# Performance work log

Measured on AMD Instinct MI355X. Metric: run time of the kernel, lower is better.

## Reference

```python
import jax, jax.numpy as jnp
import numpy as np

TAB_DIM = 6
C = 64
B, X, Y, Z = 2, 64, 64, 64
EPS = float(np.finfo(np.float32).eps)


def _gauss_1d(mu, sigma, size):
    # mu, sigma: (B, C) -> mask (B, C, size)
    coords = jnp.arange(size, dtype=jnp.float32)  # (size,)
    mu = mu * (size / 2.0) + (size / 2.0) - 0.5
    sigma = sigma * 3.5 + EPS
    d = (coords[None, None, :] - mu[:, :, None]) / sigma[:, :, None]
    return jnp.exp(-0.5 * d * d)


def _frob(t):
    return jnp.sqrt(jnp.sum(t * t))


def setup_inputs() -> dict:
    key = jax.random.key(0)
    ks = jax.random.split(key, 10)
    h = C // 2
    def lin(k, fan_in, fan_out):
        bound = 1.0 / np.sqrt(fan_in)
        kw, kb = jax.random.split(k)
        w = jax.random.uniform(kw, (fan_out, fan_in), jnp.float32, -bound, bound)
        b = jax.random.uniform(kb, (fan_out,), jnp.float32, -bound, bound)
        return w, b
    w1, b1 = lin(ks[0], TAB_DIM, h)
    w2, b2 = lin(ks[1], h, h)
    wp, bp = lin(ks[2], h, 5 * C)
    ws, bs = lin(ks[3], h, 3 * C)
    x = jax.random.normal(ks[4], (B, C, X, Y, Z), jnp.float32)
    tab = jax.random.normal(ks[5], (B, TAB_DIM), jnp.float32)
    return {"x": x, "tab": tab, "w1": w1, "b1": b1, "w2": w2, "b2": b2,
            "wp": wp, "bp": bp, "ws": ws, "bs": bs}


def reference(x, tab, w1, b1, w2, b2, wp, bp, ws, bs):
    # hypernetwork (tiny MLPs)
    emb = jnp.tanh(tab @ w1.T + b1)
    emb = jnp.tanh(emb @ w2.T + b2)
    p = emb @ wp.T + bp                     # (B, 5C)
    s = jax.nn.sigmoid(emb @ ws.T + bs)     # (B, 3C)
    scale = p[..., :C]
    shift = p[..., C:2 * C]
    mu_a = jnp.tanh(p[..., 2 * C:3 * C])
    mu_b = jnp.tanh(p[..., 3 * C:4 * C])
    mu_c = jnp.tanh(p[..., 4 * C:])
    sigma_a = s[..., :C]
    sigma_b = s[..., C:2 * C]
    sigma_c = s[..., 2 * C:]

    l2 = _frob(scale) + _frob(shift) + _frob(sigma_a) + _frob(sigma_b) + _frob(sigma_c)

    _, _, sx, sy, sz = x.shape
    gx = _gauss_1d(mu_a, sigma_a, sx)  # (B, C, X)
    gy = _gauss_1d(mu_b, sigma_b, sy)  # (B, C, Y)
    gz = _gauss_1d(mu_c, sigma_c, sz)  # (B, C, Z)

    # rank-1 outer product over X,Y,Z == the chained matmuls in torch
    a = gx[:, :, :, None, None] * gy[:, :, None, :, None] * gz[:, :, None, None, :]

    out = (1.0 - scale)[:, :, None, None, None] * x * a + shift[:, :, None, None, None]
    return out, l2
```

## Files before the change

### kernel.cpp

```cpp
#include <hip/hip_runtime.h>
#include <math.h>

#define EPSF 1.1920929e-07f

typedef float f4 __attribute__((ext_vector_type(4)));

__device__ __forceinline__ float sigmoidf_(float v) { return 1.0f / (1.0f + expf(-v)); }

__global__ void __launch_bounds__(256) fused_kernel(
        const float* __restrict__ xin, const float* __restrict__ tab,
        const float* __restrict__ w1,  const float* __restrict__ b1,
        const float* __restrict__ w2,  const float* __restrict__ b2,
        const float* __restrict__ wp,  const float* __restrict__ bp,
        const float* __restrict__ wsg, const float* __restrict__ bsg,
        float* __restrict__ out, int out_last)
{
    __shared__ float emb1[2][32];
    __shared__ float emb2[2][32];
    __shared__ float head[8];
    __shared__ float gys[64], gzs[64];
    __shared__ float pv_sh, sh_sh;

    const int blk = blockIdx.x;
    const int bc  = blk >> 6;
    const int xi  = blk & 63;
    const int b   = bc >> 6;
    const int c   = bc & 63;
    const int tid = threadIdx.x;

    if (tid < 64) {
        int bb = tid >> 5, j = tid & 31;
        float acc = b1[j];
        #pragma unroll
        for (int k = 0; k < 6; ++k) acc += tab[bb * 6 + k] * w1[j * 6 + k];
        emb1[bb][j] = tanhf(acc);
    }
    __syncthreads();

    if (tid < 64) {
        int bb = tid >> 5, j = tid & 31;
        float acc = b2[j];
        #pragma unroll
        for (int k = 0; k < 32; ++k) acc += emb1[bb][k] * w2[j * 32 + k];
        emb2[bb][j] = tanhf(acc);
    }
    __syncthreads();

    if (tid < 8) {
        const float* W  = (tid < 5) ? wp  : wsg;
        const float* Bv = (tid < 5) ? bp  : bsg;
        int row = ((tid < 5) ? tid : (tid - 5)) * 64 + c;
        float acc = Bv[row];
        #pragma unroll
        for (int k = 0; k < 32; ++k) acc += emb2[b][k] * W[row * 32 + k];
        head[tid] = acc;
    }
    __syncthreads();

    if (tid < 64) {
        float m  = tanhf(head[3]) * 32.0f + 31.5f;
        float sg = sigmoidf_(head[6]) * 3.5f + EPSF;
        float d  = ((float)tid - m) / sg;
        gys[tid] = expf(-0.5f * d * d);
    } else if (tid < 128) {
        int i = tid - 64;
        float m  = tanhf(head[4]) * 32.0f + 31.5f;
        float sg = sigmoidf_(head[7]) * 3.5f + EPSF;
        float d  = ((float)i - m) / sg;
        gzs[i] = expf(-0.5f * d * d);
    } else if (tid == 128) {
        float m  = tanhf(head[2]) * 32.0f + 31.5f;
        float sg = sigmoidf_(head[5]) * 3.5f + EPSF;
        float d  = ((float)xi - m) / sg;
        pv_sh = (1.0f - head[0]) * expf(-0.5f * d * d);
        sh_sh = head[1];
    }

    if (blk == 0) {
        __shared__ float sq[5][128];
        for (int t = tid; t < 640; t += 256) {
            int q = t / 128, r = t % 128;
            int bb = r >> 6, cc = r & 63;
            const float* W  = (q < 2) ? wp  : wsg;
            const float* Bv = (q < 2) ? bp  : bsg;
            int row = ((q < 2) ? q : (q - 2)) * 64 + cc;
            float acc = Bv[row];
            #pragma unroll
            for (int k = 0; k < 32; ++k) acc += emb2[bb][k] * W[row * 32 + k];
            if (q >= 2) acc = sigmoidf_(acc);
            sq[q][r] = acc * acc;
        }
        __syncthreads();
        if (tid == 0) {
            float tot = 0.0f;
            for (int q = 0; q < 5; ++q) {
                float ssum = 0.0f;
                for (int i = 0; i < 128; ++i) ssum += sq[q][i];
                tot += sqrtf(ssum);
            }
            out[out_last] = tot;
        }
    }
    __syncthreads();

    const float pv = pv_sh;
    const float sh = sh_sh;
    const f4* x4 = (const f4*)(xin + (size_t)blk * 4096);
    f4*       o4 = (f4*)(out + (size_t)blk * 4096);

    #pragma unroll
    for (int k = 0; k < 4; ++k) {
        int i4 = tid + k * 256;
        int y  = i4 >> 4;
        int z0 = (i4 & 15) << 2;
        f4 xv = __builtin_nontemporal_load(&x4[i4]);
        float m = pv * gys[y];
        f4 ov;
        ov.x = fmaf(m * gzs[z0 + 0], xv.x, sh);
        ov.y = fmaf(m * gzs[z0 + 1], xv.y, sh);
        ov.z = fmaf(m * gzs[z0 + 2], xv.z, sh);
        ov.w = fmaf(m * gzs[z0 + 3], xv.w, sh);
        __builtin_nontemporal_store(ov, &o4[i4]);
    }
}

extern "C" void kernel_launch(void* const* d_in, const int* in_sizes, int n_in,
                              void* d_out, int out_size, void* d_ws, size_t ws_size,
                              hipStream_t stream)
{
    const float* x   = (const float*)d_in[0];
    const float* tab = (const float*)d_in[1];
    const float* w1  = (const float*)d_in[2];
    const float* b1  = (const float*)d_in[3];
    const float* w2  = (const float*)d_in[4];
    const float* b2  = (const float*)d_in[5];
    const float* wp  = (const float*)d_in[6];
    const float* bp  = (const float*)d_in[7];
    const float* wsg = (const float*)d_in[8];
    const float* bsg = (const float*)d_in[9];

    float* out = (float*)d_out;

    fused_kernel<<<2 * 64 * 64, 256, 0, stream>>>(
        x, tab, w1, b1, w2, b2, wp, bp, wsg, bsg, out, out_size - 1);
}
```

Baseline: 49.48 us.

## Split hypernetwork setup into separate kernel and precompute gaussian tables

```diff
diff --git a/kernel.cpp b/kernel.cpp
--- a/kernel.cpp
+++ b/kernel.cpp
@@ -7,24 +7,23 @@
 
 __device__ __forceinline__ float sigmoidf_(float v) { return 1.0f / (1.0f + expf(-v)); }
 
-__global__ void __launch_bounds__(256) fused_kernel(
-        const float* __restrict__ xin, const float* __restrict__ tab,
+__global__ void __launch_bounds__(256) setup_kernel(
+        const float* __restrict__ tab,
         const float* __restrict__ w1,  const float* __restrict__ b1,
         const float* __restrict__ w2,  const float* __restrict__ b2,
         const float* __restrict__ wp,  const float* __restrict__ bp,
         const float* __restrict__ wsg, const float* __restrict__ bsg,
+        float* __restrict__ pvt, float* __restrict__ sht,
+        f4* __restrict__ gy4T, f4* __restrict__ gz4t,
         float* __restrict__ out, int out_last)
 {
     __shared__ float emb1[2][32];
     __shared__ float emb2[2][32];
     __shared__ float head[8];
     __shared__ float gys[64], gzs[64];
-    __shared__ float pv_sh, sh_sh;
 
-    const int blk = blockIdx.x;
-    const int bc  = blk >> 6;
-    const int xi  = blk & 63;
-    const int b   = bc >> 6;
+    const int bc  = blockIdx.x;
+    const int b   = (bc >> 6) & 1;
     const int c   = bc & 63;
     const int tid = threadIdx.x;
 
@@ -45,6 +44,33 @@
         emb2[bb][j] = tanhf(acc);
     }
     __syncthreads();
+
+    if (bc == 128) {
+        __shared__ float sq[5][128];
+        for (int t = tid; t < 640; t += 256) {
+            int q = t / 128, r = t % 128;
+            int bb = r >> 6, cc = r & 63;
+            const float* W  = (q < 2) ? wp  : wsg;
+            const float* Bv = (q < 2) ? bp  : bsg;
+            int row = ((q < 2) ? q : (q - 2)) * 64 + cc;
+            float acc = Bv[row];
+            #pragma unroll
+            for (int k = 0; k < 32; ++k) acc += emb2[bb][k] * W[row * 32 + k];
+            if (q >= 2) acc = sigmoidf_(acc);
+            sq[q][r] = acc * acc;
+        }
+        __syncthreads();
+        if (tid == 0) {
+            float tot = 0.0f;
+            for (int q = 0; q < 5; ++q) {
+                float ssum = 0.0f;
+                for (int i = 0; i < 128; ++i) ssum += sq[q][i];
+                tot += sqrtf(ssum);
+            }
+            out[out_last] = tot;
+        }
+        return;
+    }
 
     if (tid < 8) {
         const float* W  = (tid < 5) ? wp  : wsg;
@@ -68,60 +94,60 @@
         float sg = sigmoidf_(head[7]) * 3.5f + EPSF;
         float d  = ((float)i - m) / sg;
         gzs[i] = expf(-0.5f * d * d);
-    } else if (tid == 128) {
-        float m  = tanhf(head[2]) * 32.0f + 31.5f;
-        float sg = sigmoidf_(head[5]) * 3.5f + EPSF;
-        float d  = ((float)xi - m) / sg;
-        pv_sh = (1.0f - head[0]) * expf(-0.5f * d * d);
-        sh_sh = head[1];
-    }
-
-    if (blk == 0) {
-        __shared__ float sq[5][128];
-        for (int t = tid; t < 640; t += 256) {
-            int q = t / 128, r = t % 128;
-            int bb = r >> 6, cc = r & 63;
-            const float* W  = (q < 2) ? wp  : wsg;
-            const float* Bv = (q < 2) ? bp  : bsg;
-            int row = ((q < 2) ? q : (q - 2)) * 64 + cc;
-            float acc = Bv[row];
-            #pragma unroll
-            for (int k = 0; k < 32; ++k) acc += emb2[bb][k] * W[row * 32 + k];
-            if (q >= 2) acc = sigmoidf_(acc);
-            sq[q][r] = acc * acc;
-        }
-        __syncthreads();
-        if (tid == 0) {
-            float tot = 0.0f;
-            for (int q = 0; q < 5; ++q) {
-                float ssum = 0.0f;
-                for (int i = 0; i < 128; ++i) ssum += sq[q][i];
-                tot += sqrtf(ssum);
-            }
-            out[out_last] = tot;
-        }
     }
     __syncthreads();
 
-    const float pv = pv_sh;
-    const float sh = sh_sh;
+    if (tid < 64) {
+        float m  = tanhf(head[2]) * 32.0f + 31.5f;
+        float sg = sigmoidf_(head[5]) * 3.5f + EPSF;
+        float d  = ((float)tid - m) / sg;
+        pvt[bc * 64 + tid] = (1.0f - head[0]) * expf(-0.5f * d * d);
+    } else if (tid < 80) {
+        int t = tid - 64;
+        f4 v = {gys[t], gys[t + 16], gys[t + 32], gys[t + 48]};
+        gy4T[bc * 16 + t] = v;
+    } else if (tid < 96) {
+        int t = tid - 80;
+        f4 v = {gzs[4 * t], gzs[4 * t + 1], gzs[4 * t + 2], gzs[4 * t + 3]};
+        gz4t[bc * 16 + t] = v;
+    } else if (tid == 96) {
+        sht[bc] = head[1];
+    }
+}
+
+__global__ void __launch_bounds__(256) apply_kernel(
+        const float* __restrict__ xin,
+        const float* __restrict__ pvt, const float* __restrict__ sht,
+        const f4* __restrict__ gy4T, const f4* __restrict__ gz4t,
+        float* __restrict__ out)
+{
+    const int blk = blockIdx.x;
+    const int bc  = blk >> 6;
+    const int tid = threadIdx.x;
+
     const f4* x4 = (const f4*)(xin + (size_t)blk * 4096);
     f4*       o4 = (f4*)(out + (size_t)blk * 4096);
 
-    #pragma unroll
-    for (int k = 0; k < 4; ++k) {
-        int i4 = tid + k * 256;
-        int y  = i4 >> 4;
-        int z0 = (i4 & 15) << 2;
-        f4 xv = __builtin_nontemporal_load(&x4[i4]);
-        float m = pv * gys[y];
-        f4 ov;
-        ov.x = fmaf(m * gzs[z0 + 0], xv.x, sh);
-        ov.y = fmaf(m * gzs[z0 + 1], xv.y, sh);
-        ov.z = fmaf(m * gzs[z0 + 2], xv.z, sh);
-        ov.w = fmaf(m * gzs[z0 + 3], xv.w, sh);
-        __builtin_nontemporal_store(ov, &o4[i4]);
-    }
+    f4 x0 = x4[tid];
+    f4 x1 = x4[tid + 256];
+    f4 x2 = x4[tid + 512];
+    f4 x3 = x4[tid + 768];
+
+    const float pv  = pvt[blk];
+    const float sh  = sht[bc];
+    const f4    gyv = gy4T[bc * 16 + (tid >> 4)];
+    const f4    vz  = gz4t[bc * 16 + (tid & 15)];
+
+    const f4 w0 = vz * (pv * gyv.x);
+    const f4 w1 = vz * (pv * gyv.y);
+    const f4 w2 = vz * (pv * gyv.z);
+    const f4 w3 = vz * (pv * gyv.w);
+    const f4 shv = {sh, sh, sh, sh};
+
+    o4[tid]       = w0 * x0 + shv;
+    o4[tid + 256] = w1 * x1 + shv;
+    o4[tid + 512] = w2 * x2 + shv;
+    o4[tid + 768] = w3 * x3 + shv;
 }
 
 extern "C" void kernel_launch(void* const* d_in, const int* in_sizes, int n_in,
@@ -139,8 +165,16 @@
     const float* wsg = (const float*)d_in[8];
     const float* bsg = (const float*)d_in[9];
 
+    float* ws   = (float*)d_ws;
+    float* pvt  = ws;
+    float* sht  = ws + 8192;
+    f4*    gy4T = (f4*)(ws + 8320);
+    f4*    gz4t = (f4*)(ws + 16512);
+
     float* out = (float*)d_out;
 
-    fused_kernel<<<2 * 64 * 64, 256, 0, stream>>>(
-        x, tab, w1, b1, w2, b2, wp, bp, wsg, bsg, out, out_size - 1);
+    setup_kernel<<<129, 256, 0, stream>>>(tab, w1, b1, w2, b2, wp, bp, wsg, bsg,
+                                          pvt, sht, gy4T, gz4t, out, out_size - 1);
+
+    apply_kernel<<<2 * 64 * 64, 256, 0, stream>>>(x, pvt, sht, gy4T, gz4t, out);
 }
```

After: 53.61 us. 8.4% more time.
